# Kernel optimization log

Measured on AMD Instinct MI355X. Metric: run time of the kernel, lower is better.

## Reference

```python
import jax, jax.numpy as jnp
import numpy as np

N = 1024      # nodes (fully connected graph -> N^2 edges)
D = 3         # spatial dim
H_DIM = 64    # node feature dim
MSG = 64      # edge message dim
HID = 128     # MLP hidden dim


def _linear_init(key, fan_in, fan_out):
    k1, k2 = jax.random.split(key)
    s = 1.0 / np.sqrt(fan_in)
    w = jax.random.uniform(k1, (fan_in, fan_out), minval=-s, maxval=s, dtype=jnp.float32)
    b = jax.random.uniform(k2, (fan_out,), minval=-s, maxval=s, dtype=jnp.float32)
    return w, b


def setup_inputs() -> dict:
    key = jax.random.key(0)
    kx, kh, ke1, ke2, kn1, kn2, kc1, kc2 = jax.random.split(key, 8)
    x = jax.random.normal(kx, (N, D), dtype=jnp.float32)
    h = jax.random.normal(kh, (N, H_DIM), dtype=jnp.float32)
    # edge_mlp: (2*h_dim + 1) -> HID -> MSG
    ew1, eb1 = _linear_init(ke1, 2 * H_DIM + 1, HID)
    ew2, eb2 = _linear_init(ke2, HID, MSG)
    # node_mlp: (h_dim + msg) -> HID -> h_dim
    nw1, nb1 = _linear_init(kn1, H_DIM + MSG, HID)
    nw2, nb2 = _linear_init(kn2, HID, H_DIM)
    # coord_mlp: msg -> HID -> 1
    cw1, cb1 = _linear_init(kc1, MSG, HID)
    cw2, cb2 = _linear_init(kc2, HID, 1)
    return {"x": x, "h": h,
            "ew1": ew1, "eb1": eb1, "ew2": ew2, "eb2": eb2,
            "nw1": nw1, "nb1": nb1, "nw2": nw2, "nb2": nb2,
            "cw1": cw1, "cb1": cb1, "cw2": cw2, "cb2": cb2}


def _mlp2(inp, w1, b1, w2, b2):
    # depth-2 MLP: Linear -> SiLU -> Linear (no output activation)
    return jax.nn.silu(inp @ w1 + b1) @ w2 + b2


def reference(x, h, ew1, eb1, ew2, eb2, nw1, nb1, nw2, nb2, cw1, cb1, cw2, cb2):
    n = x.shape[0]
    # pairwise displacement and squared distance: (N,N,D), (N,N,1)
    dx = x[:, None, :] - x[None, :, :]
    r2 = jnp.sum(dx * dx, axis=-1, keepdims=True)
    hd = h.shape[-1]
    h_i = jnp.broadcast_to(h[:, None, :], (n, n, hd))
    h_j = jnp.broadcast_to(h[None, :, :], (n, n, hd))
    edge_in = jnp.concatenate([h_i, h_j, r2], axis=-1)      # (N,N,2H+1)
    m_ij = _mlp2(edge_in, ew1, eb1, ew2, eb2)               # (N,N,MSG)
    not_self = 1.0 - jnp.eye(n, dtype=x.dtype)
    m_ij = m_ij * not_self[:, :, None]
    phi_ij = _mlp2(m_ij, cw1, cb1, cw2, cb2)                # (N,N,1)
    x_update = jnp.sum(dx * phi_ij, axis=1) / (n - 1 + 1e-08)
    x_new = x + x_update
    m_i = jnp.sum(m_ij, axis=1)                             # (N,MSG)
    node_in = jnp.concatenate([h, m_i], axis=-1)            # (N,H+MSG)
    dh = _mlp2(node_in, nw1, nb1, nw2, nb2)                 # (N,H)
    h_new = h + dh  # residual_h = True
    return (x_new, h_new)
```

## Files before the change

### kernel.cpp

```cpp
#include <hip/hip_runtime.h>
#include <hip/hip_bf16.h>

#define NN   1024
#define HD   64
#define MSGD 64
#define HIDD 128

typedef __attribute__((ext_vector_type(4))) float f4;
typedef __attribute__((ext_vector_type(2))) float f2;
typedef __attribute__((ext_vector_type(8))) __bf16 bf16x8;
typedef __attribute__((ext_vector_type(4))) float f32x4;
typedef __attribute__((ext_vector_type(4))) unsigned int u32x4;
typedef unsigned short ushort_t;

__device__ __forceinline__ float silu_f(float v) {
    float e = __expf(-v);
    return v * __builtin_amdgcn_rcpf(1.0f + e);
}

__device__ __forceinline__ ushort_t to_bf16_bits(float v) {
    return __builtin_bit_cast(ushort_t, (__bf16)v);
}

__global__ void egnn_pre(const float* __restrict__ h, const float* __restrict__ ew1,
                         const float* __restrict__ eb1, const float* __restrict__ ew2,
                         const float* __restrict__ cw1,
                         float* __restrict__ Ah, float* __restrict__ Bh,
                         ushort_t* __restrict__ ew2f, ushort_t* __restrict__ cw1f)
{
    const int b = blockIdx.x, tid = threadIdx.x;
    if (b < 128) {
        const int n = b * 8 + (tid >> 5);
        const int c = (tid & 31) * 4;
        f4 a = *(const f4*)&eb1[c];
        f4 bb = (f4){0.f, 0.f, 0.f, 0.f};
        const float* hrow = h + n * HD;
        #pragma unroll 4
        for (int d = 0; d < HD; ++d) {
            const float hv = hrow[d];
            const f4 w1 = *(const f4*)&ew1[d * HIDD + c];
            const f4 w2 = *(const f4*)&ew1[(HD + d) * HIDD + c];
            a += hv * w1;
            bb += hv * w2;
        }
        *(f4*)&Ah[n * HIDD + c] = a;
        *(f4*)&Bh[n * HIDD + c] = bb;
    } else if (b == 128) {
        #pragma unroll
        for (int uu = 0; uu < 4; ++uu) {
            const int fl = uu * 256 + tid;
            const int f = fl >> 6, lane = fl & 63;
            const int ks = f >> 2, nt = f & 3, lq = lane >> 4, lr = lane & 15;
            float vals[8];
            #pragma unroll
            for (int e = 0; e < 8; ++e)
                vals[e] = ew2[(ks * 32 + lq * 8 + e) * MSGD + nt * 16 + lr];
            u32x4 pk;
            #pragma unroll
            for (int p = 0; p < 4; ++p)
                pk[p] = (unsigned)to_bf16_bits(vals[2 * p]) |
                        ((unsigned)to_bf16_bits(vals[2 * p + 1]) << 16);
            *(u32x4*)&ew2f[fl * 8] = pk;
        }
    } else {
        #pragma unroll
        for (int uu = 0; uu < 4; ++uu) {
            const int fl = uu * 256 + tid;
            const int f = fl >> 6, lane = fl & 63;
            const int ks = f >> 3, nt = f & 7, lq = lane >> 4, lr = lane & 15;
            float vals[8];
            #pragma unroll
            for (int e = 0; e < 8; ++e)
                vals[e] = cw1[(ks * 32 + lq * 8 + e) * HIDD + nt * 16 + lr];
            u32x4 pk;
            #pragma unroll
            for (int p = 0; p < 4; ++p)
                pk[p] = (unsigned)to_bf16_bits(vals[2 * p]) |
                        ((unsigned)to_bf16_bits(vals[2 * p + 1]) << 16);
            *(u32x4*)&cw1f[fl * 8] = pk;
        }
    }
}

__global__ __launch_bounds__(256, 2) void egnn_edge(
    const float* __restrict__ x, const float* __restrict__ wr_row,
    const float* __restrict__ Ah, const float* __restrict__ Bh,
    const ushort_t* __restrict__ ew2f, const ushort_t* __restrict__ cw1f,
    const float* __restrict__ eb2, const float* __restrict__ cb1,
    const float* __restrict__ cw2, const float* __restrict__ cb2,
    float* __restrict__ m_part, float* __restrict__ xu_part)
{
    __shared__ ushort_t ew2_lds[16][512];
    __shared__ ushort_t cw1_lds[16][512];
    __shared__ float    bh_lds[32][132];
    __shared__ ushort_t m_lds[4][32][72];
    __shared__ float    ah_lds[4][132];
    __shared__ float    xj_lds[32][4];
    __shared__ float    r2_lds[4][32];

    const int tid = threadIdx.x;
    const int w = tid >> 6, lane = tid & 63, lq = lane >> 4, lr = lane & 15;
    const int i0 = blockIdx.x * 4;
    const int jh = blockIdx.y;
    const int i = i0 + w;

    {
        const u32x4* s1 = (const u32x4*)ew2f;
        const u32x4* s2 = (const u32x4*)cw1f;
        u32x4* d1 = (u32x4*)&ew2_lds[0][0];
        u32x4* d2 = (u32x4*)&cw1_lds[0][0];
        #pragma unroll
        for (int uu = 0; uu < 4; ++uu) {
            const int idx = uu * 256 + tid;
            d1[idx] = s1[idx];
            d2[idx] = s2[idx];
        }
        const int r = tid >> 6, c = (tid & 63) * 2;
        const f2 v = *(const f2*)&Ah[(i0 + r) * HIDD + c];
        ah_lds[r][c] = v[0];
        ah_lds[r][c + 1] = v[1];
    }

    float cb1v[8], cw2v[8], eb2v[4];
    #pragma unroll
    for (int nt = 0; nt < 8; ++nt) { cb1v[nt] = cb1[nt * 16 + lr]; cw2v[nt] = cw2[nt * 16 + lr]; }
    #pragma unroll
    for (int nt = 0; nt < 4; ++nt) eb2v[nt] = eb2[nt * 16 + lr];
    const float cb2s = cb2[0];
    const float xi0 = x[i * 3 + 0], xi1 = x[i * 3 + 1], xi2 = x[i * 3 + 2];

    float m_acc[4] = {0.f, 0.f, 0.f, 0.f};
    float xq0 = 0.f, xq1 = 0.f, xq2 = 0.f;

    for (int jc = 0; jc < 16; ++jc) {
        const int j0 = jh * 512 + jc * 32;
        __syncthreads();
        #pragma unroll
        for (int uu = 0; uu < 4; ++uu) {
            const int idx = uu * 256 + tid;
            const int row = idx >> 5, c4 = (idx & 31) * 4;
            const f4 v = *(const f4*)&Bh[(j0 + row) * HIDD + c4];
            *(f4*)&bh_lds[row][c4] = v;
        }
        if (tid < 96) {
            const int r = tid / 3, c = tid - 3 * r;
            xj_lds[r][c] = x[(j0 + r) * 3 + c];
        }
        __syncthreads();
        if (lane < 32) {
            const float d0 = xi0 - xj_lds[lane][0];
            const float d1 = xi1 - xj_lds[lane][1];
            const float d2 = xi2 - xj_lds[lane][2];
            r2_lds[w][lane] = d0 * d0 + d1 * d1 + d2 * d2;
        }

        f32x4 accm[2][4];
        #pragma unroll
        for (int mt = 0; mt < 2; ++mt)
            #pragma unroll
            for (int nt = 0; nt < 4; ++nt)
                accm[mt][nt] = (f32x4){0.f, 0.f, 0.f, 0.f};

        #pragma unroll
        for (int ks = 0; ks < 4; ++ks) {
            const int kb = ks * 32 + lq * 8;
            const f4 wr0 = *(const f4*)&wr_row[kb];
            const f4 wr1 = *(const f4*)&wr_row[kb + 4];
            const f4 a0 = *(const f4*)&ah_lds[w][kb];
            const f4 a1 = *(const f4*)&ah_lds[w][kb + 4];
            bf16x8 aS[2];
            #pragma unroll
            for (int mt = 0; mt < 2; ++mt) {
                const int jl = mt * 16 + lr;
                const float r2v = r2_lds[w][jl];
                const f4 b0 = *(const f4*)&bh_lds[jl][kb];
                const f4 b1 = *(const f4*)&bh_lds[jl][kb + 4];
                #pragma unroll
                for (int e = 0; e < 4; ++e) {
                    const float s0 = silu_f(a0[e] + b0[e] + r2v * wr0[e]);
                    const float s1 = silu_f(a1[e] + b1[e] + r2v * wr1[e]);
                    aS[mt][e] = (__bf16)s0;
                    aS[mt][e + 4] = (__bf16)s1;
                }
            }
            #pragma unroll
            for (int nt = 0; nt < 4; ++nt) {
                const bf16x8 bfr = *(const bf16x8*)&ew2_lds[ks * 4 + nt][lane * 8];
                accm[0][nt] = __builtin_amdgcn_mfma_f32_16x16x32_bf16(aS[0], bfr, accm[0][nt], 0, 0, 0);
                accm[1][nt] = __builtin_amdgcn_mfma_f32_16x16x32_bf16(aS[1], bfr, accm[1][nt], 0, 0, 0);
            }
        }
        #pragma unroll
        for (int mt = 0; mt < 2; ++mt)
            #pragma unroll
            for (int nt = 0; nt < 4; ++nt)
                #pragma unroll
                for (int r = 0; r < 4; ++r)
                    accm[mt][nt][r] += eb2v[nt];
        if (i0 >= j0 && i0 < j0 + 32) {
            #pragma unroll
            for (int mt = 0; mt < 2; ++mt)
                #pragma unroll
                for (int r = 0; r < 4; ++r) {
                    const bool self = (j0 + mt * 16 + lq * 4 + r) == i;
                    #pragma unroll
                    for (int nt = 0; nt < 4; ++nt)
                        accm[mt][nt][r] = self ? 0.f : accm[mt][nt][r];
                }
        }
        #pragma unroll
        for (int mt = 0; mt < 2; ++mt)
            #pragma unroll
            for (int nt = 0; nt < 4; ++nt)
                #pragma unroll
                for (int r = 0; r < 4; ++r) {
                    const float mv = accm[mt][nt][r];
                    m_acc[nt] += mv;
                    m_lds[w][mt * 16 + lq * 4 + r][nt * 16 + lr] = to_bf16_bits(mv);
                }

        float phip[2][4];
        #pragma unroll
        for (int mt = 0; mt < 2; ++mt)
            #pragma unroll
            for (int r = 0; r < 4; ++r)
                phip[mt][r] = 0.f;

        #pragma unroll
        for (int nh = 0; nh < 2; ++nh) {
            f32x4 acct[2][4];
            #pragma unroll
            for (int mt = 0; mt < 2; ++mt)
                #pragma unroll
                for (int nt = 0; nt < 4; ++nt)
                    acct[mt][nt] = (f32x4){0.f, 0.f, 0.f, 0.f};
            #pragma unroll
            for (int ks = 0; ks < 2; ++ks) {
                bf16x8 aM[2];
                #pragma unroll
                for (int mt = 0; mt < 2; ++mt)
                    aM[mt] = *(const bf16x8*)&m_lds[w][mt * 16 + lr][ks * 32 + lq * 8];
                #pragma unroll
                for (int nt = 0; nt < 4; ++nt) {
                    const bf16x8 bfr = *(const bf16x8*)&cw1_lds[ks * 8 + nh * 4 + nt][lane * 8];
                    acct[0][nt] = __builtin_amdgcn_mfma_f32_16x16x32_bf16(aM[0], bfr, acct[0][nt], 0, 0, 0);
                    acct[1][nt] = __builtin_amdgcn_mfma_f32_16x16x32_bf16(aM[1], bfr, acct[1][nt], 0, 0, 0);
                }
            }
            #pragma unroll
            for (int mt = 0; mt < 2; ++mt)
                #pragma unroll
                for (int nt = 0; nt < 4; ++nt)
                    #pragma unroll
                    for (int r = 0; r < 4; ++r) {
                        const float tt = acct[mt][nt][r] + cb1v[nh * 4 + nt];
                        phip[mt][r] += silu_f(tt) * cw2v[nh * 4 + nt];
                    }
        }
        #pragma unroll
        for (int d = 1; d < 16; d <<= 1)
            #pragma unroll
            for (int mt = 0; mt < 2; ++mt)
                #pragma unroll
                for (int r = 0; r < 4; ++r)
                    phip[mt][r] += __shfl_xor(phip[mt][r], d);
        #pragma unroll
        for (int mt = 0; mt < 2; ++mt)
            #pragma unroll
            for (int r = 0; r < 4; ++r) {
                const int jl = mt * 16 + lq * 4 + r;
                const float phi = (lr == 0) ? (phip[mt][r] + cb2s) : 0.f;
                xq0 += (xi0 - xj_lds[jl][0]) * phi;
                xq1 += (xi1 - xj_lds[jl][1]) * phi;
                xq2 += (xi2 - xj_lds[jl][2]) * phi;
            }
    }

    #pragma unroll
    for (int nt = 0; nt < 4; ++nt) {
        m_acc[nt] += __shfl_xor(m_acc[nt], 16);
        m_acc[nt] += __shfl_xor(m_acc[nt], 32);
    }
    if (lane < 16) {
        #pragma unroll
        for (int nt = 0; nt < 4; ++nt)
            m_part[(jh * NN + i) * MSGD + nt * 16 + lane] = m_acc[nt];
    }
    #pragma unroll
    for (int d = 1; d < 64; d <<= 1) {
        xq0 += __shfl_xor(xq0, d);
        xq1 += __shfl_xor(xq1, d);
        xq2 += __shfl_xor(xq2, d);
    }
    if (lane == 0) {
        float* dst = &xu_part[(jh * NN + i) * 3];
        dst[0] = xq0; dst[1] = xq1; dst[2] = xq2;
    }
}

__global__ void egnn_node(const float* __restrict__ x, const float* __restrict__ h,
                          const float* __restrict__ nw1, const float* __restrict__ nb1,
                          const float* __restrict__ nw2, const float* __restrict__ nb2,
                          const float* __restrict__ m_part, const float* __restrict__ xu_part,
                          float* __restrict__ out)
{
    __shared__ float nin[8][132];
    __shared__ float zl[8][132];
    const int tid = threadIdx.x;
    const int r0 = blockIdx.x * 8;
    #pragma unroll
    for (int uu = 0; uu < 4; ++uu) {
        const int idx = uu * 256 + tid;
        const int row = idx >> 7, c = idx & 127;
        float v;
        if (c < 64) v = h[(r0 + row) * HD + c];
        else v = m_part[(r0 + row) * MSGD + (c - 64)] + m_part[(NN + r0 + row) * MSGD + (c - 64)];
        nin[row][c] = v;
    }
    __syncthreads();
    const int row = tid >> 5, cg = tid & 31;
    {
        const int c0 = cg * 4;
        f4 acc = *(const f4*)&nb1[c0];
        for (int k = 0; k < 128; ++k) {
            const float v = nin[row][k];
            const f4 wv = *(const f4*)&nw1[k * HIDD + c0];
            acc += v * wv;
        }
        #pragma unroll
        for (int e = 0; e < 4; ++e) zl[row][c0 + e] = silu_f(acc[e]);
    }
    __syncthreads();
    {
        const int c0 = cg * 2;
        f2 acc = *(const f2*)&nb2[c0];
        for (int k = 0; k < 128; ++k) {
            const float v = zl[row][k];
            const f2 wv = *(const f2*)&nw2[k * HD + c0];
            acc += v * wv;
        }
        const int n = r0 + row;
        const f2 hv = *(const f2*)&h[n * HD + c0];
        *(f2*)&out[3072 + n * HD + c0] = hv + acc;
    }
    if (tid < 24) {
        const int r = tid / 3, c = tid - 3 * r;
        const int n = r0 + r;
        const float xu = xu_part[n * 3 + c] + xu_part[(NN + n) * 3 + c];
        out[n * 3 + c] = x[n * 3 + c] + xu * (1.0f / 1023.0f);
    }
}

extern "C" void kernel_launch(void* const* d_in, const int* in_sizes, int n_in,
                              void* d_out, int out_size, void* d_ws, size_t ws_size,
                              hipStream_t stream)
{
    const float* x   = (const float*)d_in[0];
    const float* h   = (const float*)d_in[1];
    const float* ew1 = (const float*)d_in[2];
    const float* eb1 = (const float*)d_in[3];
    const float* ew2 = (const float*)d_in[4];
    const float* eb2 = (const float*)d_in[5];
    const float* nw1 = (const float*)d_in[6];
    const float* nb1 = (const float*)d_in[7];
    const float* nw2 = (const float*)d_in[8];
    const float* nb2 = (const float*)d_in[9];
    const float* cw1 = (const float*)d_in[10];
    const float* cb1 = (const float*)d_in[11];
    const float* cw2 = (const float*)d_in[12];
    const float* cb2 = (const float*)d_in[13];
    float* out = (float*)d_out;

    char* ws = (char*)d_ws;
    float*    Ah      = (float*)(ws);
    float*    Bh      = (float*)(ws + 524288);
    ushort_t* ew2f    = (ushort_t*)(ws + 1048576);
    ushort_t* cw1f    = (ushort_t*)(ws + 1048576 + 16384);
    float*    m_part  = (float*)(ws + 1048576 + 32768);
    float*    xu_part = (float*)(ws + 1048576 + 32768 + 524288);

    egnn_pre<<<dim3(130), dim3(256), 0, stream>>>(h, ew1, eb1, ew2, cw1, Ah, Bh, ew2f, cw1f);
    egnn_edge<<<dim3(256, 2), dim3(256), 0, stream>>>(
        x, ew1 + 128 * HIDD, Ah, Bh, ew2f, cw1f, eb2, cb1, cw2, cb2, m_part, xu_part);
    egnn_node<<<dim3(128), dim3(256), 0, stream>>>(x, h, nw1, nb1, nw2, nb2, m_part, xu_part, out);
}
```

Before: 213.0 us.

## Switch edge kernel to transposed 32x32x16 MFMA with register-resident message fragments

The edge kernel now computes transposed products (weights as the A operand, edges as B) using 32x32x16 bf16 MFMAs. This lets the message tile be rebuilt in registers through lane shuffles instead of passing through an LDS round-trip, and the coord-MLP weights are read straight from global memory rather than staged in LDS. The j dimension is split four ways instead of two, and launch bounds move to 4 waves per SIMD for more blocks and occupancy. The cost is more partial sums for the node kernel to reduce and higher register pressure from the 16-wide accumulators.

```diff
diff --git a/kernel.cpp b/kernel.cpp
--- a/kernel.cpp
+++ b/kernel.cpp
@@ -9,7 +9,7 @@
 typedef __attribute__((ext_vector_type(4))) float f4;
 typedef __attribute__((ext_vector_type(2))) float f2;
 typedef __attribute__((ext_vector_type(8))) __bf16 bf16x8;
-typedef __attribute__((ext_vector_type(4))) float f32x4;
+typedef __attribute__((ext_vector_type(16))) float f32x16;
 typedef __attribute__((ext_vector_type(4))) unsigned int u32x4;
 typedef unsigned short ushort_t;
 
@@ -21,276 +21,259 @@
 __device__ __forceinline__ ushort_t to_bf16_bits(float v) {
     return __builtin_bit_cast(ushort_t, (__bf16)v);
 }
+
+__device__ __forceinline__ unsigned pack2(float a, float b) {
+    return (unsigned)to_bf16_bits(a) | ((unsigned)to_bf16_bits(b) << 16);
+}
+
+#define ZERO16 {0.f,0.f,0.f,0.f,0.f,0.f,0.f,0.f,0.f,0.f,0.f,0.f,0.f,0.f,0.f,0.f}
 
 __global__ void egnn_pre(const float* __restrict__ h, const float* __restrict__ ew1,
                          const float* __restrict__ eb1, const float* __restrict__ ew2,
                          const float* __restrict__ cw1,
                          float* __restrict__ Ah, float* __restrict__ Bh,
-                         ushort_t* __restrict__ ew2f, ushort_t* __restrict__ cw1f)
+                         ushort_t* __restrict__ ew2tf, ushort_t* __restrict__ cw1tf)
 {
     const int b = blockIdx.x, tid = threadIdx.x;
-    if (b < 128) {
-        const int n = b * 8 + (tid >> 5);
-        const int c = (tid & 31) * 4;
-        f4 a = *(const f4*)&eb1[c];
-        f4 bb = (f4){0.f, 0.f, 0.f, 0.f};
+    if (b < 256) {
+        const int n = b * 4 + (tid >> 6);
+        const int c = (tid & 63) * 2;
+        f2 a = *(const f2*)&eb1[c];
+        f2 bb = (f2){0.f, 0.f};
         const float* hrow = h + n * HD;
         #pragma unroll 4
         for (int d = 0; d < HD; ++d) {
             const float hv = hrow[d];
-            const f4 w1 = *(const f4*)&ew1[d * HIDD + c];
-            const f4 w2 = *(const f4*)&ew1[(HD + d) * HIDD + c];
+            const f2 w1 = *(const f2*)&ew1[d * HIDD + c];
+            const f2 w2 = *(const f2*)&ew1[(HD + d) * HIDD + c];
             a += hv * w1;
             bb += hv * w2;
         }
-        *(f4*)&Ah[n * HIDD + c] = a;
-        *(f4*)&Bh[n * HIDD + c] = bb;
-    } else if (b == 128) {
+        *(f2*)&Ah[n * HIDD + c] = a;
+        *(f2*)&Bh[n * HIDD + c] = bb;
+    } else if (b == 256) {
         #pragma unroll
         for (int uu = 0; uu < 4; ++uu) {
             const int fl = uu * 256 + tid;
-            const int f = fl >> 6, lane = fl & 63;
-            const int ks = f >> 2, nt = f & 3, lq = lane >> 4, lr = lane & 15;
-            float vals[8];
-            #pragma unroll
-            for (int e = 0; e < 8; ++e)
-                vals[e] = ew2[(ks * 32 + lq * 8 + e) * MSGD + nt * 16 + lr];
+            const int f = fl >> 6, l = fl & 63;
+            const int mt = f >> 3, ks = f & 7;
+            const int msg = mt * 32 + (l & 31);
+            const int hidb = ks * 16 + (l >> 5) * 8;
             u32x4 pk;
             #pragma unroll
             for (int p = 0; p < 4; ++p)
-                pk[p] = (unsigned)to_bf16_bits(vals[2 * p]) |
-                        ((unsigned)to_bf16_bits(vals[2 * p + 1]) << 16);
-            *(u32x4*)&ew2f[fl * 8] = pk;
+                pk[p] = pack2(ew2[(hidb + 2 * p) * MSGD + msg],
+                              ew2[(hidb + 2 * p + 1) * MSGD + msg]);
+            *(u32x4*)&ew2tf[fl * 8] = pk;
         }
     } else {
         #pragma unroll
         for (int uu = 0; uu < 4; ++uu) {
             const int fl = uu * 256 + tid;
-            const int f = fl >> 6, lane = fl & 63;
-            const int ks = f >> 3, nt = f & 7, lq = lane >> 4, lr = lane & 15;
-            float vals[8];
-            #pragma unroll
-            for (int e = 0; e < 8; ++e)
-                vals[e] = cw1[(ks * 32 + lq * 8 + e) * HIDD + nt * 16 + lr];
+            const int f = fl >> 6, l = fl & 63;
+            const int mt = f >> 2, k = f & 3;
+            const int hid = mt * 32 + (l & 31);
+            const int msgb = k * 16 + (l >> 5) * 8;
             u32x4 pk;
             #pragma unroll
             for (int p = 0; p < 4; ++p)
-                pk[p] = (unsigned)to_bf16_bits(vals[2 * p]) |
-                        ((unsigned)to_bf16_bits(vals[2 * p + 1]) << 16);
-            *(u32x4*)&cw1f[fl * 8] = pk;
-        }
-    }
-}
-
-__global__ __launch_bounds__(256, 2) void egnn_edge(
+                pk[p] = pack2(cw1[(msgb + 2 * p) * HIDD + hid],
+                              cw1[(msgb + 2 * p + 1) * HIDD + hid]);
+            *(u32x4*)&cw1tf[fl * 8] = pk;
+        }
+    }
+}
+
+__global__ __launch_bounds__(256, 4) void egnn_edge(
     const float* __restrict__ x, const float* __restrict__ wr_row,
     const float* __restrict__ Ah, const float* __restrict__ Bh,
-    const ushort_t* __restrict__ ew2f, const ushort_t* __restrict__ cw1f,
+    const ushort_t* __restrict__ ew2tf, const ushort_t* __restrict__ cw1tf,
     const float* __restrict__ eb2, const float* __restrict__ cb1,
     const float* __restrict__ cw2, const float* __restrict__ cb2,
     float* __restrict__ m_part, float* __restrict__ xu_part)
 {
-    __shared__ ushort_t ew2_lds[16][512];
-    __shared__ ushort_t cw1_lds[16][512];
+    __shared__ ushort_t ew2t_lds[16][512];
     __shared__ float    bh_lds[32][132];
-    __shared__ ushort_t m_lds[4][32][72];
-    __shared__ float    ah_lds[4][132];
+    __shared__ float    ah_lds[4][128];
+    __shared__ float    wr_lds[128];
+    __shared__ float    cb1_lds[128];
+    __shared__ float    cw2_lds[128];
+    __shared__ float    eb2_lds[64];
     __shared__ float    xj_lds[32][4];
-    __shared__ float    r2_lds[4][32];
 
     const int tid = threadIdx.x;
-    const int w = tid >> 6, lane = tid & 63, lq = lane >> 4, lr = lane & 15;
-    const int i0 = blockIdx.x * 4;
-    const int jh = blockIdx.y;
+    const int w = tid >> 6, lane = tid & 63;
+    const int j32 = lane & 31, hi = lane >> 5;
+    const int i0 = blockIdx.x * 4, jh = blockIdx.y;
     const int i = i0 + w;
 
     {
-        const u32x4* s1 = (const u32x4*)ew2f;
-        const u32x4* s2 = (const u32x4*)cw1f;
-        u32x4* d1 = (u32x4*)&ew2_lds[0][0];
-        u32x4* d2 = (u32x4*)&cw1_lds[0][0];
-        #pragma unroll
-        for (int uu = 0; uu < 4; ++uu) {
-            const int idx = uu * 256 + tid;
-            d1[idx] = s1[idx];
-            d2[idx] = s2[idx];
-        }
+        const u32x4* s1 = (const u32x4*)ew2tf;
+        u32x4* d1 = (u32x4*)&ew2t_lds[0][0];
+        #pragma unroll
+        for (int uu = 0; uu < 4; ++uu) d1[uu * 256 + tid] = s1[uu * 256 + tid];
         const int r = tid >> 6, c = (tid & 63) * 2;
-        const f2 v = *(const f2*)&Ah[(i0 + r) * HIDD + c];
-        ah_lds[r][c] = v[0];
-        ah_lds[r][c + 1] = v[1];
-    }
-
-    float cb1v[8], cw2v[8], eb2v[4];
-    #pragma unroll
-    for (int nt = 0; nt < 8; ++nt) { cb1v[nt] = cb1[nt * 16 + lr]; cw2v[nt] = cw2[nt * 16 + lr]; }
-    #pragma unroll
-    for (int nt = 0; nt < 4; ++nt) eb2v[nt] = eb2[nt * 16 + lr];
+        *(f2*)&ah_lds[r][c] = *(const f2*)&Ah[(i0 + r) * HIDD + c];
+        if (tid < 128) {
+            wr_lds[tid]  = wr_row[tid];
+            cb1_lds[tid] = cb1[tid];
+            cw2_lds[tid] = cw2[tid];
+            if (tid < 64) eb2_lds[tid] = eb2[tid];
+        }
+    }
     const float cb2s = cb2[0];
     const float xi0 = x[i * 3 + 0], xi1 = x[i * 3 + 1], xi2 = x[i * 3 + 2];
 
-    float m_acc[4] = {0.f, 0.f, 0.f, 0.f};
+    f4 macc[2][4];
+    #pragma unroll
+    for (int mt = 0; mt < 2; ++mt)
+        #pragma unroll
+        for (int g = 0; g < 4; ++g) macc[mt][g] = (f4){0.f, 0.f, 0.f, 0.f};
     float xq0 = 0.f, xq1 = 0.f, xq2 = 0.f;
 
-    for (int jc = 0; jc < 16; ++jc) {
-        const int j0 = jh * 512 + jc * 32;
+    for (int jc = 0; jc < 8; ++jc) {
+        const int j0 = jh * 256 + jc * 32;
         __syncthreads();
         #pragma unroll
         for (int uu = 0; uu < 4; ++uu) {
-            const int idx = uu * 256 + tid;
-            const int row = idx >> 5, c4 = (idx & 31) * 4;
-            const f4 v = *(const f4*)&Bh[(j0 + row) * HIDD + c4];
-            *(f4*)&bh_lds[row][c4] = v;
-        }
-        if (tid < 96) {
-            const int r = tid / 3, c = tid - 3 * r;
-            xj_lds[r][c] = x[(j0 + r) * 3 + c];
+            const int idx = uu * 256 + tid, row = idx >> 5, c4 = (idx & 31) * 4;
+            *(f4*)&bh_lds[row][c4] = *(const f4*)&Bh[(j0 + row) * HIDD + c4];
+        }
+        if (tid < 128) {
+            const int r = tid >> 2, c = tid & 3;
+            xj_lds[r][c] = (c < 3) ? x[(j0 + r) * 3 + c] : 0.f;
         }
         __syncthreads();
-        if (lane < 32) {
-            const float d0 = xi0 - xj_lds[lane][0];
-            const float d1 = xi1 - xj_lds[lane][1];
-            const float d2 = xi2 - xj_lds[lane][2];
-            r2_lds[w][lane] = d0 * d0 + d1 * d1 + d2 * d2;
-        }
-
-        f32x4 accm[2][4];
+
+        const f4 xj = *(const f4*)&xj_lds[j32][0];
+        const float d0 = xi0 - xj[0], d1v = xi1 - xj[1], d2v = xi2 - xj[2];
+        const float r2 = d0 * d0 + d1v * d1v + d2v * d2v;
+
+        f32x16 accA = ZERO16, accB = ZERO16;
+        #pragma unroll
+        for (int ks = 0; ks < 8; ++ks) {
+            const int hidb = ks * 16 + hi * 8;
+            const f4 a0 = *(const f4*)&ah_lds[w][hidb];
+            const f4 a1 = *(const f4*)&ah_lds[w][hidb + 4];
+            const f4 w0 = *(const f4*)&wr_lds[hidb];
+            const f4 w1 = *(const f4*)&wr_lds[hidb + 4];
+            const f4 b0 = *(const f4*)&bh_lds[j32][hidb];
+            const f4 b1 = *(const f4*)&bh_lds[j32][hidb + 4];
+            bf16x8 sf;
+            #pragma unroll
+            for (int e = 0; e < 4; ++e) {
+                sf[e]     = (__bf16)silu_f(fmaf(r2, w0[e], a0[e]) + b0[e]);
+                sf[e + 4] = (__bf16)silu_f(fmaf(r2, w1[e], a1[e]) + b1[e]);
+            }
+            const bf16x8 af0 = *(const bf16x8*)&ew2t_lds[ks][lane * 8];
+            const bf16x8 af1 = *(const bf16x8*)&ew2t_lds[8 + ks][lane * 8];
+            accA = __builtin_amdgcn_mfma_f32_32x32x16_bf16(af0, sf, accA, 0, 0, 0);
+            accB = __builtin_amdgcn_mfma_f32_32x32x16_bf16(af1, sf, accB, 0, 0, 0);
+        }
+
+        const bool has_self = (i >= j0) && (i < j0 + 32);
+        const bool is_self = has_self && ((j0 + j32) == i);
+        unsigned pk0[8], pk1[8];
+        #pragma unroll
+        for (int g = 0; g < 4; ++g) {
+            f4 qa, qb;
+            #pragma unroll
+            for (int rr = 0; rr < 4; ++rr) { qa[rr] = accA[g * 4 + rr]; qb[rr] = accB[g * 4 + rr]; }
+            const f4 ea = *(const f4*)&eb2_lds[8 * g + 4 * hi];
+            const f4 eb = *(const f4*)&eb2_lds[32 + 8 * g + 4 * hi];
+            qa += ea; qb += eb;
+            #pragma unroll
+            for (int rr = 0; rr < 4; ++rr) {
+                qa[rr] = is_self ? 0.f : qa[rr];
+                qb[rr] = is_self ? 0.f : qb[rr];
+            }
+            macc[0][g] += qa; macc[1][g] += qb;
+            pk0[g * 2]     = pack2(qa[0], qa[1]);
+            pk0[g * 2 + 1] = pack2(qa[2], qa[3]);
+            pk1[g * 2]     = pack2(qb[0], qb[1]);
+            pk1[g * 2 + 1] = pack2(qb[2], qb[3]);
+        }
+
+        bf16x8 mfrag[4];
+        #pragma unroll
+        for (int k = 0; k < 4; ++k) {
+            unsigned lo0, lo1, hh0, hh1;
+            {
+                constexpr_helper:;
+            }
+            {
+                const int M = 2 * k;
+                lo0 = (M >> 2) ? pk1[(M & 3) * 2] : pk0[(M & 3) * 2];
+                lo1 = (M >> 2) ? pk1[(M & 3) * 2 + 1] : pk0[(M & 3) * 2 + 1];
+            }
+            {
+                const int M = 2 * k + 1;
+                hh0 = (M >> 2) ? pk1[(M & 3) * 2] : pk0[(M & 3) * 2];
+                hh1 = (M >> 2) ? pk1[(M & 3) * 2 + 1] : pk0[(M & 3) * 2 + 1];
+            }
+            const unsigned own0 = hi ? hh0 : lo0, own1 = hi ? hh1 : lo1;
+            const unsigned snd0 = hi ? lo0 : hh0, snd1 = hi ? lo1 : hh1;
+            const unsigned rcv0 = __shfl_xor(snd0, 32), rcv1 = __shfl_xor(snd1, 32);
+            u32x4 fr;
+            fr[0] = hi ? rcv0 : own0;
+            fr[1] = hi ? rcv1 : own1;
+            fr[2] = hi ? own0 : rcv0;
+            fr[3] = hi ? own1 : rcv1;
+            mfrag[k] = __builtin_bit_cast(bf16x8, fr);
+        }
+
+        float phi = 0.f;
+        #pragma unroll
+        for (int half = 0; half < 2; ++half) {
+            f32x16 t0 = ZERO16, t1 = ZERO16;
+            #pragma unroll
+            for (int k = 0; k < 4; ++k) {
+                const bf16x8 A0 = *(const bf16x8*)&cw1tf[(((half * 2 + 0) * 4 + k) * 64 + lane) * 8];
+                const bf16x8 A1 = *(const bf16x8*)&cw1tf[(((half * 2 + 1) * 4 + k) * 64 + lane) * 8];
+                t0 = __builtin_amdgcn_mfma_f32_32x32x16_bf16(A0, mfrag[k], t0, 0, 0, 0);
+                t1 = __builtin_amdgcn_mfma_f32_32x32x16_bf16(A1, mfrag[k], t1, 0, 0, 0);
+            }
+            #pragma unroll
+            for (int g = 0; g < 4; ++g) {
+                const int hb0 = (half * 2 + 0) * 32 + 8 * g + 4 * hi;
+                const int hb1 = (half * 2 + 1) * 32 + 8 * g + 4 * hi;
+                const f4 c10 = *(const f4*)&cb1_lds[hb0];
+                const f4 c20 = *(const f4*)&cw2_lds[hb0];
+                const f4 c11 = *(const f4*)&cb1_lds[hb1];
+                const f4 c21 = *(const f4*)&cw2_lds[hb1];
+                #pragma unroll
+                for (int rr = 0; rr < 4; ++rr) {
+                    phi += silu_f(t0[g * 4 + rr] + c10[rr]) * c20[rr];
+                    phi += silu_f(t1[g * 4 + rr] + c11[rr]) * c21[rr];
+                }
+            }
+        }
+        phi += __shfl_xor(phi, 32);
+        phi = (phi + cb2s) * 0.5f;
+        xq0 += d0 * phi; xq1 += d1v * phi; xq2 += d2v * phi;
+    }
+
+    #pragma unroll
+    for (int mask = 1; mask <= 16; mask <<= 1)
         #pragma unroll
         for (int mt = 0; mt < 2; ++mt)
             #pragma unroll
-            for (int nt = 0; nt < 4; ++nt)
-                accm[mt][nt] = (f32x4){0.f, 0.f, 0.f, 0.f};
-
-        #pragma unroll
-        for (int ks = 0; ks < 4; ++ks) {
-            const int kb = ks * 32 + lq * 8;
-            const f4 wr0 = *(const f4*)&wr_row[kb];
-            const f4 wr1 = *(const f4*)&wr_row[kb + 4];
-            const f4 a0 = *(const f4*)&ah_lds[w][kb];
-            const f4 a1 = *(const f4*)&ah_lds[w][kb + 4];
-            bf16x8 aS[2];
-            #pragma unroll
-            for (int mt = 0; mt < 2; ++mt) {
-                const int jl = mt * 16 + lr;
-                const float r2v = r2_lds[w][jl];
-                const f4 b0 = *(const f4*)&bh_lds[jl][kb];
-                const f4 b1 = *(const f4*)&bh_lds[jl][kb + 4];
+            for (int g = 0; g < 4; ++g)
                 #pragma unroll
-                for (int e = 0; e < 4; ++e) {
-                    const float s0 = silu_f(a0[e] + b0[e] + r2v * wr0[e]);
-                    const float s1 = silu_f(a1[e] + b1[e] + r2v * wr1[e]);
-                    aS[mt][e] = (__bf16)s0;
-                    aS[mt][e + 4] = (__bf16)s1;
-                }
-            }
-            #pragma unroll
-            for (int nt = 0; nt < 4; ++nt) {
-                const bf16x8 bfr = *(const bf16x8*)&ew2_lds[ks * 4 + nt][lane * 8];
-                accm[0][nt] = __builtin_amdgcn_mfma_f32_16x16x32_bf16(aS[0], bfr, accm[0][nt], 0, 0, 0);
-                accm[1][nt] = __builtin_amdgcn_mfma_f32_16x16x32_bf16(aS[1], bfr, accm[1][nt], 0, 0, 0);
-            }
-        }
+                for (int rr = 0; rr < 4; ++rr)
+                    macc[mt][g][rr] += __shfl_xor(macc[mt][g][rr], mask);
+    if (j32 == 0) {
         #pragma unroll
         for (int mt = 0; mt < 2; ++mt)
             #pragma unroll
-            for (int nt = 0; nt < 4; ++nt)
-                #pragma unroll
-                for (int r = 0; r < 4; ++r)
-                    accm[mt][nt][r] += eb2v[nt];
-        if (i0 >= j0 && i0 < j0 + 32) {
-            #pragma unroll
-            for (int mt = 0; mt < 2; ++mt)
-                #pragma unroll
-                for (int r = 0; r < 4; ++r) {
-                    const bool self = (j0 + mt * 16 + lq * 4 + r) == i;
-                    #pragma unroll
-                    for (int nt = 0; nt < 4; ++nt)
-                        accm[mt][nt][r] = self ? 0.f : accm[mt][nt][r];
-                }
-        }
-        #pragma unroll
-        for (int mt = 0; mt < 2; ++mt)
-            #pragma unroll
-            for (int nt = 0; nt < 4; ++nt)
-                #pragma unroll
-                for (int r = 0; r < 4; ++r) {
-                    const float mv = accm[mt][nt][r];
-                    m_acc[nt] += mv;
-                    m_lds[w][mt * 16 + lq * 4 + r][nt * 16 + lr] = to_bf16_bits(mv);
-                }
-
-        float phip[2][4];
-        #pragma unroll
-        for (int mt = 0; mt < 2; ++mt)
-            #pragma unroll
-            for (int r = 0; r < 4; ++r)
-                phip[mt][r] = 0.f;
-
-        #pragma unroll
-        for (int nh = 0; nh < 2; ++nh) {
-            f32x4 acct[2][4];
-            #pragma unroll
-            for (int mt = 0; mt < 2; ++mt)
-                #pragma unroll
-                for (int nt = 0; nt < 4; ++nt)
-                    acct[mt][nt] = (f32x4){0.f, 0.f, 0.f, 0.f};
-            #pragma unroll
-            for (int ks = 0; ks < 2; ++ks) {
-                bf16x8 aM[2];
-                #pragma unroll
-                for (int mt = 0; mt < 2; ++mt)
-                    aM[mt] = *(const bf16x8*)&m_lds[w][mt * 16 + lr][ks * 32 + lq * 8];
-                #pragma unroll
-                for (int nt = 0; nt < 4; ++nt) {
-                    const bf16x8 bfr = *(const bf16x8*)&cw1_lds[ks * 8 + nh * 4 + nt][lane * 8];
-                    acct[0][nt] = __builtin_amdgcn_mfma_f32_16x16x32_bf16(aM[0], bfr, acct[0][nt], 0, 0, 0);
-                    acct[1][nt] = __builtin_amdgcn_mfma_f32_16x16x32_bf16(aM[1], bfr, acct[1][nt], 0, 0, 0);
-                }
-            }
-            #pragma unroll
-            for (int mt = 0; mt < 2; ++mt)
-                #pragma unroll
-                for (int nt = 0; nt < 4; ++nt)
-                    #pragma unroll
-                    for (int r = 0; r < 4; ++r) {
-                        const float tt = acct[mt][nt][r] + cb1v[nh * 4 + nt];
-                        phip[mt][r] += silu_f(tt) * cw2v[nh * 4 + nt];
-                    }
-        }
-        #pragma unroll
-        for (int d = 1; d < 16; d <<= 1)
-            #pragma unroll
-            for (int mt = 0; mt < 2; ++mt)
-                #pragma unroll
-                for (int r = 0; r < 4; ++r)
-                    phip[mt][r] += __shfl_xor(phip[mt][r], d);
-        #pragma unroll
-        for (int mt = 0; mt < 2; ++mt)
-            #pragma unroll
-            for (int r = 0; r < 4; ++r) {
-                const int jl = mt * 16 + lq * 4 + r;
-                const float phi = (lr == 0) ? (phip[mt][r] + cb2s) : 0.f;
-                xq0 += (xi0 - xj_lds[jl][0]) * phi;
-                xq1 += (xi1 - xj_lds[jl][1]) * phi;
-                xq2 += (xi2 - xj_lds[jl][2]) * phi;
-            }
-    }
-
+            for (int g = 0; g < 4; ++g)
+                *(f4*)&m_part[(jh * NN + i) * MSGD + mt * 32 + 8 * g + 4 * hi] = macc[mt][g];
+    }
     #pragma unroll
-    for (int nt = 0; nt < 4; ++nt) {
-        m_acc[nt] += __shfl_xor(m_acc[nt], 16);
-        m_acc[nt] += __shfl_xor(m_acc[nt], 32);
-    }
-    if (lane < 16) {
-        #pragma unroll
-        for (int nt = 0; nt < 4; ++nt)
-            m_part[(jh * NN + i) * MSGD + nt * 16 + lane] = m_acc[nt];
-    }
-    #pragma unroll
-    for (int d = 1; d < 64; d <<= 1) {
-        xq0 += __shfl_xor(xq0, d);
-        xq1 += __shfl_xor(xq1, d);
-        xq2 += __shfl_xor(xq2, d);
+    for (int mask = 1; mask <= 32; mask <<= 1) {
+        xq0 += __shfl_xor(xq0, mask);
+        xq1 += __shfl_xor(xq1, mask);
+        xq2 += __shfl_xor(xq2, mask);
     }
     if (lane == 0) {
         float* dst = &xu_part[(jh * NN + i) * 3];
@@ -314,7 +297,13 @@
         const int row = idx >> 7, c = idx & 127;
         float v;
         if (c < 64) v = h[(r0 + row) * HD + c];
-        else v = m_part[(r0 + row) * MSGD + (c - 64)] + m_part[(NN + r0 + row) * MSGD + (c - 64)];
+        else {
+            const int cc = c - 64;
+            v = m_part[(r0 + row) * MSGD + cc]
+              + m_part[(NN + r0 + row) * MSGD + cc]
+              + m_part[(2 * NN + r0 + row) * MSGD + cc]
+              + m_part[(3 * NN + r0 + row) * MSGD + cc];
+        }
         nin[row][c] = v;
     }
     __syncthreads();
@@ -346,7 +335,8 @@
     if (tid < 24) {
         const int r = tid / 3, c = tid - 3 * r;
         const int n = r0 + r;
-        const float xu = xu_part[n * 3 + c] + xu_part[(NN + n) * 3 + c];
+        const float xu = xu_part[n * 3 + c] + xu_part[(NN + n) * 3 + c]
+                       + xu_part[(2 * NN + n) * 3 + c] + xu_part[(3 * NN + n) * 3 + c];
         out[n * 3 + c] = x[n * 3 + c] + xu * (1.0f / 1023.0f);
     }
 }
@@ -373,14 +363,14 @@
 
     char* ws = (char*)d_ws;
     float*    Ah      = (float*)(ws);
-    float*    Bh      = (float*)(ws + 524288);
-    ushort_t* ew2f    = (ushort_t*)(ws + 1048576);
-    ushort_t* cw1f    = (ushort_t*)(ws + 1048576 + 16384);
-    float*    m_part  = (float*)(ws + 1048576 + 32768);
-    float*    xu_part = (float*)(ws + 1048576 + 32768 + 524288);
-
-    egnn_pre<<<dim3(130), dim3(256), 0, stream>>>(h, ew1, eb1, ew2, cw1, Ah, Bh, ew2f, cw1f);
-    egnn_edge<<<dim3(256, 2), dim3(256), 0, stream>>>(
-        x, ew1 + 128 * HIDD, Ah, Bh, ew2f, cw1f, eb2, cb1, cw2, cb2, m_part, xu_part);
+    float*    Bh      = (float*)(ws + (512 << 10));
+    ushort_t* ew2tf   = (ushort_t*)(ws + (1024 << 10));
+    ushort_t* cw1tf   = (ushort_t*)(ws + (1040 << 10));
+    float*    m_part  = (float*)(ws + (1056 << 10));
+    float*    xu_part = (float*)(ws + (2080 << 10));
+
+    egnn_pre<<<dim3(258), dim3(256), 0, stream>>>(h, ew1, eb1, ew2, cw1, Ah, Bh, ew2tf, cw1tf);
+    egnn_edge<<<dim3(256, 4), dim3(256), 0, stream>>>(
+        x, ew1 + 128 * HIDD, Ah, Bh, ew2tf, cw1tf, eb2, cb1, cw2, cb2, m_part, xu_part);
     egnn_node<<<dim3(128), dim3(256), 0, stream>>>(x, h, nw1, nb1, nw2, nb2, m_part, xu_part, out);
 }
```

After: 312.5 us. +46.8%, slower.
